# Kernel tuning notes

Hardware: AMD Instinct MI355X
Metric: run time of the kernel (lower is better)

The kernel has to match this reference:

```python
import jax, jax.numpy as jnp
import numpy as np
from jax import lax

B, S, D_IN, D_H, D_R = 4, 4096, 1024, 2048, 256

def setup_inputs() -> dict:
    key = jax.random.key(0)
    ks = jax.random.split(key, 8)
    def xavier(k, shape):
        fan_in, fan_out = shape[1], shape[0]
        lim = np.sqrt(6.0 / (fan_in + fan_out))
        return jax.random.uniform(k, shape, jnp.float32, -lim, lim)
    return {
        "x": jax.random.normal(ks[0], (B, S, D_IN), jnp.float32),
        "hidden": jnp.zeros((B, D_H), jnp.float32),
        "W_delta": xavier(ks[1], (D_R, D_IN + D_H)),            # delta_proj (no bias)
        "W_expand": xavier(ks[2], (D_H, D_R)),                   # delta_expand
        "b_expand": jnp.zeros((D_H,), jnp.float32),
        "W_gate": xavier(ks[3], (D_H, D_IN + D_H)),              # gate_proj
        "b_gate": jnp.ones((D_H,), jnp.float32),                 # init constant 1.0
        "W_value": xavier(ks[4], (D_H, D_IN)),                   # value_proj
        "b_value": jnp.zeros((D_H,), jnp.float32),
    }

def reference(x, hidden, W_delta, W_expand, b_expand, W_gate, b_gate, W_value, b_value):
    act = jax.nn.silu
    # v_t = act(value_proj(x_t))  -> (B, S, D_H)
    v = act(jnp.einsum('bsi,hi->bsh', x, W_value) + b_value)
    # NOTE: faithful to the torch parallel-scan path, the "previous hidden"
    # used for delta/gate is the INITIAL hidden h0 broadcast to all timesteps.
    h_prev = jnp.broadcast_to(hidden[:, None, :], (x.shape[0], x.shape[1], hidden.shape[-1]))
    combined = jnp.concatenate([x, h_prev], axis=-1)             # (B, S, D_IN+D_H)
    delta_latent = jnp.einsum('bsc,rc->bsr', combined, W_delta)  # (B, S, D_R)
    delta = jnp.einsum('bsr,hr->bsh', act(delta_latent), W_expand) + b_expand
    gate = jax.nn.sigmoid(jnp.einsum('bsc,hc->bsh', combined, W_gate) + b_gate)
    a = 1.0 - gate                                               # (B, S, D_H)
    b = gate * (v + delta)
    # fold initial state into first step: h_1 = a_1 * h0 + b_1
    b = b.at[:, 0, :].add(a[:, 0, :] * hidden)
    # linear recurrence h_t = a_t * h_{t-1} + b_t via associative scan
    def combine_fn(c1, c2):
        a1, b1 = c1
        a2, b2 = c2
        return a2 * a1, a2 * b1 + b2
    _, h_all = lax.associative_scan(combine_fn, (a, b), axis=1)  # (B, S, D_H)
    return h_all, h_all[:, -1, :]
```

## Files before the change

kernel.cpp:

```cpp
#include <hip/hip_runtime.h>
#include <hip/hip_bf16.h>
#include <cstdint>

#define DIN 1024
#define DH  2048
#define DR  256
#define SEQ 4096
#define NB  4
#define MTOK (NB*SEQ)
#define NCHUNK 64
#define CL (SEQ/NCHUNK)
#define NCH (NB*DH)

typedef __attribute__((ext_vector_type(8))) short bf16x8;
typedef __attribute__((ext_vector_type(4))) float f32x4;

__device__ __forceinline__ unsigned short f2bf(float f) {
  union { float f; unsigned u; } v; v.f = f;
  unsigned r = v.u + 0x7fffu + ((v.u >> 16) & 1u);
  return (unsigned short)(r >> 16);
}

__device__ __forceinline__ float bf2f(unsigned s) {
  union { unsigned u; float f; } v; v.u = s << 16; return v.f;
}

__device__ __forceinline__ unsigned pack_ab(float a, float b) {
  return (unsigned)f2bf(a) | ((unsigned)f2bf(b) << 16);
}

__device__ __forceinline__ float sigmoidf_(float x) {
  return 1.0f / (1.0f + __expf(-x));
}

__global__ void cast_strided_kernel(const float* __restrict__ src,
                                    unsigned short* __restrict__ dst,
                                    int rows, int cols, int src_ld) {
  int cols4 = cols >> 2;
  int total = rows * cols4;
  for (int i = blockIdx.x * blockDim.x + threadIdx.x; i < total;
       i += gridDim.x * blockDim.x) {
    int r  = i / cols4;
    int c4 = i - r * cols4;
    const float4 v = *reinterpret_cast<const float4*>(src + (size_t)r * src_ld + c4 * 4);
    ushort4 o;
    o.x = f2bf(v.x); o.y = f2bf(v.y); o.z = f2bf(v.z); o.w = f2bf(v.w);
    *reinterpret_cast<ushort4*>(dst + (size_t)r * cols + c4 * 4) = o;
  }
}

__global__ void hd_kernel(const float* __restrict__ Wg, const float* __restrict__ Wd,
                          const float* __restrict__ hidden,
                          float* __restrict__ hd_gate, float* __restrict__ hd_delta) {
  int wid  = (blockIdx.x * blockDim.x + threadIdx.x) >> 6;
  int lane = threadIdx.x & 63;
  if (wid >= DH + DR) return;
  const float* wrow;
  int ch; bool isGate;
  if (wid < DH) { isGate = true;  ch = wid;      wrow = Wg + (size_t)ch * (DIN + DH) + DIN; }
  else          { isGate = false; ch = wid - DH; wrow = Wd + (size_t)ch * (DIN + DH) + DIN; }
  float acc[NB] = {0.f, 0.f, 0.f, 0.f};
  for (int k = lane; k < DH; k += 64) {
    float w = wrow[k];
    #pragma unroll
    for (int b = 0; b < NB; b++) acc[b] += w * hidden[b * DH + k];
  }
  #pragma unroll
  for (int b = 0; b < NB; b++) {
    float v = acc[b];
    #pragma unroll
    for (int off = 32; off; off >>= 1) v += __shfl_down(v, off);
    if (lane == 0) {
      if (isGate) hd_gate[b * DH + ch] = v;
      else        hd_delta[b * DR + ch] = v;
    }
  }
}

__device__ __forceinline__ void stage_async(const unsigned short* __restrict__ src,
                                            int src_ld, unsigned short* lds,
                                            int rows, int wid, int lane) {
  int r8 = lane >> 3;
  int c  = (lane & 7) ^ (r8 & 7);
  const unsigned short* g0 = src + (size_t)r8 * src_ld + c * 8;
  int nsegs = rows >> 3;
  for (int s = wid; s < nsegs; s += 4) {
    const unsigned short* g = g0 + (size_t)(s * 8) * src_ld;
    __builtin_amdgcn_global_load_lds(
        (const __attribute__((address_space(1))) void*)g,
        (__attribute__((address_space(3))) void*)(lds + s * 512),
        16, 0, 0);
  }
}

__device__ __forceinline__ bf16x8 read_frag(const unsigned short* lds, int row,
                                            int kk, int lane) {
  int c = (kk * 4 + (lane >> 4)) ^ (row & 7);
  return *reinterpret_cast<const bf16x8*>(lds + row * 64 + c * 8);
}

__global__ __launch_bounds__(256, 2) void gemm_P(
    const unsigned short* __restrict__ Xb, const unsigned short* __restrict__ Wdb,
    const float* __restrict__ hd_delta, unsigned short* __restrict__ P) {
  __shared__ __align__(16) unsigned short As[128 * 64];
  __shared__ __align__(16) unsigned short Bs[64 * 64];
  int tid = threadIdx.x, lane = tid & 63, wid = tid >> 6;
  int wm = wid >> 1, wn = wid & 1;
  int bm0 = blockIdx.x * 128;
  int bn0 = blockIdx.y * 64;
  f32x4 acc[4][2];
  #pragma unroll
  for (int m = 0; m < 4; m++)
    #pragma unroll
    for (int n = 0; n < 2; n++) acc[m][n] = (f32x4){0.f, 0.f, 0.f, 0.f};

  for (int k0 = 0; k0 < DIN; k0 += 64) {
    stage_async(Xb + (size_t)bm0 * DIN + k0, DIN, As, 128, wid, lane);
    stage_async(Wdb + (size_t)bn0 * DIN + k0, DIN, Bs, 64, wid, lane);
    __syncthreads();
    #pragma unroll
    for (int kk = 0; kk < 2; kk++) {
      bf16x8 af[4], bf[2];
      #pragma unroll
      for (int m = 0; m < 4; m++) af[m] = read_frag(As, wm * 64 + m * 16 + (lane & 15), kk, lane);
      #pragma unroll
      for (int n = 0; n < 2; n++) bf[n] = read_frag(Bs, wn * 32 + n * 16 + (lane & 15), kk, lane);
      #pragma unroll
      for (int m = 0; m < 4; m++)
        #pragma unroll
        for (int n = 0; n < 2; n++)
          acc[m][n] = __builtin_amdgcn_mfma_f32_16x16x32_bf16(af[m], bf[n], acc[m][n], 0, 0, 0);
    }
    __syncthreads();
  }
  int batch = bm0 >> 12;
  #pragma unroll
  for (int n = 0; n < 2; n++) {
    int ch = bn0 + wn * 32 + n * 16 + (lane & 15);
    float hd = hd_delta[batch * DR + ch];
    #pragma unroll
    for (int m = 0; m < 4; m++) {
      #pragma unroll
      for (int r = 0; r < 4; r++) {
        int tok = bm0 + wm * 64 + m * 16 + (lane >> 4) * 4 + r;
        float v = acc[m][n][r] + hd;
        v = v * sigmoidf_(v);
        P[(size_t)tok * DR + ch] = f2bf(v);
      }
    }
  }
}

__global__ __launch_bounds__(256, 2) void gemm_fused(
    const unsigned short* __restrict__ Xb, const unsigned short* __restrict__ Wvb,
    const unsigned short* __restrict__ Wgb, const unsigned short* __restrict__ P,
    const unsigned short* __restrict__ Web,
    const float* __restrict__ b_value, const float* __restrict__ b_gate,
    const float* __restrict__ b_expand, const float* __restrict__ hd_gate,
    unsigned* __restrict__ ws_ab) {
  __shared__ __align__(16) unsigned short As[128 * 64];
  __shared__ __align__(16) unsigned short Bv[64 * 64];
  __shared__ __align__(16) unsigned short Bg[64 * 64];
  int tid = threadIdx.x, lane = tid & 63, wid = tid >> 6;
  int wm = wid >> 1, wn = wid & 1;
  int bm0 = blockIdx.x * 128;
  int bn0 = blockIdx.y * 64;
  f32x4 acc_v[4][2], acc_g[4][2], acc_d[4][2];
  #pragma unroll
  for (int m = 0; m < 4; m++)
    #pragma unroll
    for (int n = 0; n < 2; n++) {
      acc_v[m][n] = (f32x4){0.f, 0.f, 0.f, 0.f};
      acc_g[m][n] = (f32x4){0.f, 0.f, 0.f, 0.f};
      acc_d[m][n] = (f32x4){0.f, 0.f, 0.f, 0.f};
    }

  for (int k0 = 0; k0 < DIN; k0 += 64) {
    stage_async(Xb + (size_t)bm0 * DIN + k0, DIN, As, 128, wid, lane);
    stage_async(Wvb + (size_t)bn0 * DIN + k0, DIN, Bv, 64, wid, lane);
    stage_async(Wgb + (size_t)bn0 * DIN + k0, DIN, Bg, 64, wid, lane);
    __syncthreads();
    #pragma unroll
    for (int kk = 0; kk < 2; kk++) {
      bf16x8 af[4], bvf[2], bgf[2];
      #pragma unroll
      for (int m = 0; m < 4; m++) af[m] = read_frag(As, wm * 64 + m * 16 + (lane & 15), kk, lane);
      #pragma unroll
      for (int n = 0; n < 2; n++) {
        bvf[n] = read_frag(Bv, wn * 32 + n * 16 + (lane & 15), kk, lane);
        bgf[n] = read_frag(Bg, wn * 32 + n * 16 + (lane & 15), kk, lane);
      }
      #pragma unroll
      for (int m = 0; m < 4; m++)
        #pragma unroll
        for (int n = 0; n < 2; n++) {
          acc_v[m][n] = __builtin_amdgcn_mfma_f32_16x16x32_bf16(af[m], bvf[n], acc_v[m][n], 0, 0, 0);
          acc_g[m][n] = __builtin_amdgcn_mfma_f32_16x16x32_bf16(af[m], bgf[n], acc_g[m][n], 0, 0, 0);
        }
    }
    __syncthreads();
  }
  for (int k0 = 0; k0 < DR; k0 += 64) {
    stage_async(P + (size_t)bm0 * DR + k0, DR, As, 128, wid, lane);
    stage_async(Web + (size_t)bn0 * DR + k0, DR, Bv, 64, wid, lane);
    __syncthreads();
    #pragma unroll
    for (int kk = 0; kk < 2; kk++) {
      bf16x8 af[4], bef[2];
      #pragma unroll
      for (int m = 0; m < 4; m++) af[m] = read_frag(As, wm * 64 + m * 16 + (lane & 15), kk, lane);
      #pragma unroll
      for (int n = 0; n < 2; n++) bef[n] = read_frag(Bv, wn * 32 + n * 16 + (lane & 15), kk, lane);
      #pragma unroll
      for (int m = 0; m < 4; m++)
        #pragma unroll
        for (int n = 0; n < 2; n++)
          acc_d[m][n] = __builtin_amdgcn_mfma_f32_16x16x32_bf16(af[m], bef[n], acc_d[m][n], 0, 0, 0);
    }
    __syncthreads();
  }
  int batch = bm0 >> 12;
  #pragma unroll
  for (int n = 0; n < 2; n++) {
    int ch = bn0 + wn * 32 + n * 16 + (lane & 15);
    float bv_ = b_value[ch];
    float bg_ = b_gate[ch] + hd_gate[batch * DH + ch];
    float be_ = b_expand[ch];
    #pragma unroll
    for (int m = 0; m < 4; m++) {
      #pragma unroll
      for (int r = 0; r < 4; r++) {
        int tok = bm0 + wm * 64 + m * 16 + (lane >> 4) * 4 + r;
        float vv = acc_v[m][n][r] + bv_;
        vv = vv * sigmoidf_(vv);
        float gg = sigmoidf_(acc_g[m][n][r] + bg_);
        float dd = acc_d[m][n][r] + be_;
        ws_ab[(size_t)tok * DH + ch] = pack_ab(1.0f - gg, gg * (vv + dd));
      }
    }
  }
}

__global__ __launch_bounds__(256) void scan_partials(const unsigned* __restrict__ ab,
                                                     float2* __restrict__ partial) {
  int id = blockIdx.x * 256 + threadIdx.x;
  int q = id & 4095;
  int c = id >> 12;
  int g = q * 2;
  int b = g >> 11, ch = g & 2047;
  const unsigned* p = ab + ((size_t)(b * SEQ + c * CL) * DH + ch);
  float A0 = 1.f, B0 = 0.f, A1 = 1.f, B1 = 0.f;
  #pragma unroll 8
  for (int i = 0; i < CL; i++) {
    uint2 u = *reinterpret_cast<const uint2*>(p + (size_t)i * DH);
    float a0 = bf2f(u.x & 0xffffu), b0 = bf2f(u.x >> 16);
    float a1 = bf2f(u.y & 0xffffu), b1 = bf2f(u.y >> 16);
    B0 = fmaf(a0, B0, b0); A0 *= a0;
    B1 = fmaf(a1, B1, b1); A1 *= a1;
  }
  float4 w = {A0, B0, A1, B1};
  *reinterpret_cast<float4*>(partial + (size_t)c * NCH + g) = w;
}

__global__ void scan_chunks(const float2* __restrict__ partial,
                            const float* __restrict__ hidden,
                            float* __restrict__ prefix, float* __restrict__ out) {
  int g = blockIdx.x * 256 + threadIdx.x;
  float H = hidden[g];
  for (int c = 0; c < NCHUNK; c++) {
    prefix[c * NCH + g] = H;
    float2 AB = partial[(size_t)c * NCH + g];
    H = fmaf(AB.x, H, AB.y);
  }
  out[(size_t)MTOK * DH + g] = H;
}

__global__ __launch_bounds__(256) void scan_apply(const unsigned* __restrict__ ab,
                                                  const float* __restrict__ prefix,
                                                  float* __restrict__ out) {
  int id = blockIdx.x * 256 + threadIdx.x;
  int q = id & 4095;
  int c = id >> 12;
  int g = q * 2;
  int b = g >> 11, ch = g & 2047;
  size_t base = (size_t)(b * SEQ + c * CL) * DH + ch;
  const unsigned* p = ab + base;
  float* o = out + base;
  float h0 = prefix[c * NCH + g];
  float h1 = prefix[c * NCH + g + 1];
  #pragma unroll 8
  for (int i = 0; i < CL; i++) {
    uint2 u = *reinterpret_cast<const uint2*>(p + (size_t)i * DH);
    float a0 = bf2f(u.x & 0xffffu), b0 = bf2f(u.x >> 16);
    float a1 = bf2f(u.y & 0xffffu), b1 = bf2f(u.y >> 16);
    h0 = fmaf(a0, h0, b0);
    h1 = fmaf(a1, h1, b1);
    float2 w = {h0, h1};
    *reinterpret_cast<float2*>(o + (size_t)i * DH) = w;
  }
}

extern "C" void kernel_launch(void* const* d_in, const int* in_sizes, int n_in,
                              void* d_out, int out_size, void* d_ws, size_t ws_size,
                              hipStream_t stream) {
  (void)in_sizes; (void)n_in; (void)out_size; (void)ws_size;
  const float* x      = (const float*)d_in[0];
  const float* hidden = (const float*)d_in[1];
  const float* Wd     = (const float*)d_in[2];
  const float* We     = (const float*)d_in[3];
  const float* be     = (const float*)d_in[4];
  const float* Wg     = (const float*)d_in[5];
  const float* bg     = (const float*)d_in[6];
  const float* Wv     = (const float*)d_in[7];
  const float* bv     = (const float*)d_in[8];
  float* out = (float*)d_out;
  char* ws = (char*)d_ws;

  unsigned*       ws_ab    = (unsigned*)(ws);
  unsigned short* Xb       = (unsigned short*)(ws + 134217728);
  unsigned short* Pb       = (unsigned short*)(ws + 167772160);
  unsigned short* Wvb      = (unsigned short*)(ws + 176160768);
  unsigned short* Wgb      = (unsigned short*)(ws + 180355072);
  unsigned short* Wdb      = (unsigned short*)(ws + 184549376);
  unsigned short* Web      = (unsigned short*)(ws + 185073664);
  float*          hd_gate  = (float*)(ws + 186122240);
  float*          hd_delta = (float*)(ws + 186155008);
  float2*         partial  = (float2*)(ws + 134217728);
  float*          prefix   = (float*)(ws + 138412032);

  cast_strided_kernel<<<2048, 256, 0, stream>>>(x,  Xb,  MTOK, DIN, DIN);
  cast_strided_kernel<<<512,  256, 0, stream>>>(Wv, Wvb, DH,   DIN, DIN);
  cast_strided_kernel<<<512,  256, 0, stream>>>(Wg, Wgb, DH,   DIN, DIN + DH);
  cast_strided_kernel<<<64,   256, 0, stream>>>(Wd, Wdb, DR,   DIN, DIN + DH);
  cast_strided_kernel<<<128,  256, 0, stream>>>(We, Web, DH,   DR,  DR);
  hd_kernel<<<(DH + DR) / 4, 256, 0, stream>>>(Wg, Wd, hidden, hd_gate, hd_delta);
  gemm_P<<<dim3(MTOK / 128, DR / 64), 256, 0, stream>>>(Xb, Wdb, hd_delta, Pb);
  gemm_fused<<<dim3(MTOK / 128, DH / 64), 256, 0, stream>>>(
      Xb, Wvb, Wgb, Pb, Web, bv, bg, be, hd_gate, ws_ab);
  scan_partials<<<(NCH/2) * NCHUNK / 256, 256, 0, stream>>>(ws_ab, partial);
  scan_chunks<<<NCH / 256, 256, 0, stream>>>(partial, hidden, prefix, out);
  scan_apply<<<(NCH/2) * NCHUNK / 256, 256, 0, stream>>>(ws_ab, prefix, out);
}
```

Before: 339.3 us.

## Fuse chunk-scan partials into GEMM epilogue and swizzle block order

Each gemm_fused block now reduces its 64-token chunks in registers with wave shuffles, writing per-chunk (A,B) partials directly. This removes the separate scan_partials kernel, which re-read the whole packed a/b workspace. Both GEMMs also switch to a 1D grid with a swizzled block-to-tile mapping, meant to improve L2 reuse of weight and activation tiles. Partials are now stored in the output buffer as scratch before scan_apply overwrites it, and the epilogue adds shuffles and extra registers.

```diff
diff --git a/kernel.cpp b/kernel.cpp
--- a/kernel.cpp
+++ b/kernel.cpp
@@ -106,8 +106,10 @@
   __shared__ __align__(16) unsigned short Bs[64 * 64];
   int tid = threadIdx.x, lane = tid & 63, wid = tid >> 6;
   int wm = wid >> 1, wn = wid & 1;
-  int bm0 = blockIdx.x * 128;
-  int bn0 = blockIdx.y * 64;
+  int bid = blockIdx.x;
+  int swz = (bid & 7) * 64 + (bid >> 3);
+  int bm0 = (swz & 127) * 128;
+  int bn0 = (swz >> 7) * 64;
   f32x4 acc[4][2];
   #pragma unroll
   for (int m = 0; m < 4; m++)
@@ -157,14 +159,16 @@
     const unsigned short* __restrict__ Web,
     const float* __restrict__ b_value, const float* __restrict__ b_gate,
     const float* __restrict__ b_expand, const float* __restrict__ hd_gate,
-    unsigned* __restrict__ ws_ab) {
+    unsigned* __restrict__ ws_ab, float2* __restrict__ partial) {
   __shared__ __align__(16) unsigned short As[128 * 64];
   __shared__ __align__(16) unsigned short Bv[64 * 64];
   __shared__ __align__(16) unsigned short Bg[64 * 64];
   int tid = threadIdx.x, lane = tid & 63, wid = tid >> 6;
   int wm = wid >> 1, wn = wid & 1;
-  int bm0 = blockIdx.x * 128;
-  int bn0 = blockIdx.y * 64;
+  int bid = blockIdx.x;
+  int swz = (bid & 7) * 512 + (bid >> 3);
+  int bm0 = (swz & 127) * 128;
+  int bn0 = (swz >> 7) * 64;
   f32x4 acc_v[4][2], acc_g[4][2], acc_d[4][2];
   #pragma unroll
   for (int m = 0; m < 4; m++)
@@ -220,46 +224,59 @@
     __syncthreads();
   }
   int batch = bm0 >> 12;
+  int cbase = ((bm0 & (SEQ - 1)) >> 6) + wm;
+  int q = lane >> 4;
   #pragma unroll
   for (int n = 0; n < 2; n++) {
     int ch = bn0 + wn * 32 + n * 16 + (lane & 15);
     float bv_ = b_value[ch];
     float bg_ = b_gate[ch] + hd_gate[batch * DH + ch];
     float be_ = b_expand[ch];
+    unsigned pk[4][4];
     #pragma unroll
     for (int m = 0; m < 4; m++) {
       #pragma unroll
       for (int r = 0; r < 4; r++) {
-        int tok = bm0 + wm * 64 + m * 16 + (lane >> 4) * 4 + r;
+        int tok = bm0 + wm * 64 + m * 16 + q * 4 + r;
         float vv = acc_v[m][n][r] + bv_;
         vv = vv * sigmoidf_(vv);
         float gg = sigmoidf_(acc_g[m][n][r] + bg_);
         float dd = acc_d[m][n][r] + be_;
-        ws_ab[(size_t)tok * DH + ch] = pack_ab(1.0f - gg, gg * (vv + dd));
-      }
-    }
-  }
-}
-
-__global__ __launch_bounds__(256) void scan_partials(const unsigned* __restrict__ ab,
-                                                     float2* __restrict__ partial) {
-  int id = blockIdx.x * 256 + threadIdx.x;
-  int q = id & 4095;
-  int c = id >> 12;
-  int g = q * 2;
-  int b = g >> 11, ch = g & 2047;
-  const unsigned* p = ab + ((size_t)(b * SEQ + c * CL) * DH + ch);
-  float A0 = 1.f, B0 = 0.f, A1 = 1.f, B1 = 0.f;
-  #pragma unroll 8
-  for (int i = 0; i < CL; i++) {
-    uint2 u = *reinterpret_cast<const uint2*>(p + (size_t)i * DH);
-    float a0 = bf2f(u.x & 0xffffu), b0 = bf2f(u.x >> 16);
-    float a1 = bf2f(u.y & 0xffffu), b1 = bf2f(u.y >> 16);
-    B0 = fmaf(a0, B0, b0); A0 *= a0;
-    B1 = fmaf(a1, B1, b1); A1 *= a1;
-  }
-  float4 w = {A0, B0, A1, B1};
-  *reinterpret_cast<float4*>(partial + (size_t)c * NCH + g) = w;
+        unsigned pw = pack_ab(1.0f - gg, gg * (vv + dd));
+        pk[m][r] = pw;
+        ws_ab[(size_t)tok * DH + ch] = pw;
+      }
+    }
+    float A = 1.f, B = 0.f;
+    #pragma unroll
+    for (int m = 0; m < 4; m++) {
+      float Am = 1.f, Bm = 0.f;
+      #pragma unroll
+      for (int r = 0; r < 4; r++) {
+        float ar = bf2f(pk[m][r] & 0xffffu), br = bf2f(pk[m][r] >> 16);
+        Bm = fmaf(ar, Bm, br); Am *= ar;
+      }
+      {
+        float Ao = __shfl_xor(Am, 16), Bo = __shfl_xor(Bm, 16);
+        bool hi = (lane >> 4) & 1;
+        float A1 = hi ? Ao : Am, B1 = hi ? Bo : Bm;
+        float A2 = hi ? Am : Ao, B2 = hi ? Bm : Bo;
+        Am = A2 * A1; Bm = fmaf(A2, B1, B2);
+      }
+      {
+        float Ao = __shfl_xor(Am, 32), Bo = __shfl_xor(Bm, 32);
+        bool hi = (lane >> 5) & 1;
+        float A1 = hi ? Ao : Am, B1 = hi ? Bo : Bm;
+        float A2 = hi ? Am : Ao, B2 = hi ? Bm : Bo;
+        Am = A2 * A1; Bm = fmaf(A2, B1, B2);
+      }
+      B = fmaf(Am, B, Bm); A *= Am;
+    }
+    if (lane < 16) {
+      float2 w = {A, B};
+      partial[(size_t)cbase * NCH + batch * DH + ch] = w;
+    }
+  }
 }
 
 __global__ void scan_chunks(const float2* __restrict__ partial,
@@ -325,8 +342,8 @@
   unsigned short* Web      = (unsigned short*)(ws + 185073664);
   float*          hd_gate  = (float*)(ws + 186122240);
   float*          hd_delta = (float*)(ws + 186155008);
-  float2*         partial  = (float2*)(ws + 134217728);
-  float*          prefix   = (float*)(ws + 138412032);
+  float2*         partial  = (float2*)out;
+  float*          prefix   = (float*)(ws + 134217728);
 
   cast_strided_kernel<<<2048, 256, 0, stream>>>(x,  Xb,  MTOK, DIN, DIN);
   cast_strided_kernel<<<512,  256, 0, stream>>>(Wv, Wvb, DH,   DIN, DIN);
@@ -334,10 +351,9 @@
   cast_strided_kernel<<<64,   256, 0, stream>>>(Wd, Wdb, DR,   DIN, DIN + DH);
   cast_strided_kernel<<<128,  256, 0, stream>>>(We, Web, DH,   DR,  DR);
   hd_kernel<<<(DH + DR) / 4, 256, 0, stream>>>(Wg, Wd, hidden, hd_gate, hd_delta);
-  gemm_P<<<dim3(MTOK / 128, DR / 64), 256, 0, stream>>>(Xb, Wdb, hd_delta, Pb);
-  gemm_fused<<<dim3(MTOK / 128, DH / 64), 256, 0, stream>>>(
-      Xb, Wvb, Wgb, Pb, Web, bv, bg, be, hd_gate, ws_ab);
-  scan_partials<<<(NCH/2) * NCHUNK / 256, 256, 0, stream>>>(ws_ab, partial);
+  gemm_P<<<512, 256, 0, stream>>>(Xb, Wdb, hd_delta, Pb);
+  gemm_fused<<<4096, 256, 0, stream>>>(
+      Xb, Wvb, Wgb, Pb, Web, bv, bg, be, hd_gate, ws_ab, partial);
   scan_chunks<<<NCH / 256, 256, 0, stream>>>(partial, hidden, prefix, out);
   scan_apply<<<(NCH/2) * NCHUNK / 256, 256, 0, stream>>>(ws_ab, prefix, out);
 }
```

After: 367.1 us. +8.2%, slower.
